# Performance work log

Measured on AMD Instinct MI355X. Metric: run time of the kernel, lower is better.

The kernel has to match this reference:

```python
import jax, jax.numpy as jnp
import numpy as np

B, N, T, N_IN = 4, 40, 64, 4
N_EMB, N_HID = 32, 64
EPS = 1e-05


def _spatial_rels(n):
    # fully-connected directed edges without self-loops (NRI convention)
    offdiag = np.ones((n, n)) - np.eye(n)
    recv_idx, send_idx = np.where(offdiag)[0], np.where(offdiag)[1]
    eye = np.eye(n, dtype=np.float32)
    return eye[recv_idx], eye[send_idx]  # [n*(n-1), n] each


def _temporal_rels(t):
    # all t*t ordered pairs (including self), one-hot
    eye = np.eye(t, dtype=np.float32)
    recv = np.repeat(np.arange(t), t)
    send = np.tile(np.arange(t), t)
    return eye[recv], eye[send]  # [t*t, t] each


def setup_inputs() -> dict:
    key = jax.random.key(0)
    ks = jax.random.split(key, 8)
    rel_rec, rel_send = _spatial_rels(N)
    rel_rec_t, rel_send_t = _temporal_rels(T)
    s_emb = 1.0 / np.sqrt(N_IN)
    s_lstm = 1.0 / np.sqrt(N_HID)
    s_att = 1.0 / np.sqrt(2 * N_HID)
    return {
        "inputs": jax.random.normal(ks[0], (B, N, T, N_IN), dtype=jnp.float32),
        "rel_rec": jnp.asarray(rel_rec),
        "rel_send": jnp.asarray(rel_send),
        "rel_rec_t": jnp.asarray(rel_rec_t),
        "rel_send_t": jnp.asarray(rel_send_t),
        "W_emb": jax.random.uniform(ks[1], (N_EMB, N_IN), jnp.float32, -s_emb, s_emb),
        "b_emb": jnp.zeros((N_EMB,), jnp.float32),
        "W_ih": jax.random.uniform(ks[2], (4 * N_HID, N_EMB), jnp.float32, -s_lstm, s_lstm),
        "W_hh": jax.random.uniform(ks[3], (4 * N_HID, N_HID), jnp.float32, -s_lstm, s_lstm),
        "b_ih": jax.random.uniform(ks[4], (4 * N_HID,), jnp.float32, -s_lstm, s_lstm),
        "b_hh": jax.random.uniform(ks[5], (4 * N_HID,), jnp.float32, -s_lstm, s_lstm),
        "W_att": jax.random.uniform(ks[6], (1, 2 * N_HID), jnp.float32, -s_att, s_att),
        "b_att": jnp.zeros((1,), jnp.float32),
    }


def _forward(inputs, rel_rec, rel_send, rel_rec_t, rel_send_t,
             W_emb, b_emb, W_ih, W_hh, b_ih, b_hh, W_att, b_att):
    b, n, t, _ = inputs.shape
    nh = W_hh.shape[1]
    locs = inputs[..., :2]

    # ---- LSTMEncoder: per-timestep embedding + LSTM cell (scan over time) ----
    emb = jnp.einsum("bnti,ei->bnte", inputs, W_emb) + b_emb       # [B,N,T,n_emb]
    xs = emb.transpose(2, 0, 1, 3).reshape(t, b * n, -1)            # [T,BN,n_emb]

    def step(carry, x):
        h, c = carry
        gates = x @ W_ih.T + b_ih + h @ W_hh.T + b_hh               # [BN,4H]
        i_g, f_g, g_g, o_g = jnp.split(gates, 4, axis=-1)           # torch gate order i,f,g,o
        i_g = jax.nn.sigmoid(i_g)
        f_g = jax.nn.sigmoid(f_g)
        g_g = jnp.tanh(g_g)
        o_g = jax.nn.sigmoid(o_g)
        c = f_g * c + i_g * g_g
        h = o_g * jnp.tanh(c)
        return (h, c), h

    h0 = jnp.zeros((b * n, nh), inputs.dtype)
    _, hs_t = jax.lax.scan(step, (h0, h0), xs)                      # [T,BN,H]
    hs = hs_t.transpose(1, 0, 2).reshape(b, n, t, nh)               # [B,N,T,H]

    # ---- SoftAttention over timesteps ----
    hsf = hs.reshape(b * n, t, nh)                                  # [BN,T,H]
    senders = jnp.einsum("kt,mth->mkh", rel_send_t, hsf)            # [BN,T*T,H]
    receivers = jnp.einsum("kt,mth->mkh", rel_rec_t, hsf)
    edges = jnp.concatenate([senders, receivers], axis=-1)          # [BN,T*T,2H]
    scores = jnp.einsum("mkf,of->mko", edges, W_att)[..., 0] + b_att[0]  # [BN,T*T]
    # adj = rel_send_t^T @ diag(scores) @ rel_rec_t (done without diag_embed)
    adj_s = jnp.einsum("ki,mk,kj->mij", rel_send_t, scores, rel_rec_t)   # [BN,T,T]
    adj_sn = jax.nn.softmax(adj_s, axis=-1)
    cs = jnp.einsum("mij,mjh->mih", adj_sn, hsf).reshape(b, n, t, nh)    # [B,N,T,H]

    # ---- HardwiredAttention over atoms ----
    locs_re = locs.reshape(b, n, -1)                                 # [B,N,T*2]
    snd = jnp.einsum("en,bnf->bef", rel_send, locs_re).reshape(b, -1, t, 2)
    rcv = jnp.einsum("en,bnf->bef", rel_rec, locs_re).reshape(b, -1, t, 2)
    dist = jnp.sqrt(((snd - rcv) ** 2).sum(-1))                      # [B,E,T]
    w = (1.0 / (dist + EPS)).transpose(0, 2, 1)                      # [B,T,E]
    adj_h = jnp.einsum("ei,bte,ej->btij", rel_send, w, rel_rec)      # [B,T,N,N]
    ch = jnp.einsum("btij,btjh->btih", adj_h, hs.transpose(0, 2, 1, 3))
    ch = ch.transpose(0, 2, 1, 3)                                    # [B,N,T,H]

    c_out = jnp.tanh(jnp.concatenate([cs[:, :, -1, :], ch.sum(2)], axis=-1))  # [B,N,2H]
    return c_out


def reference(inputs, rel_rec, rel_send, rel_rec_t, rel_send_t,
              W_emb, b_emb, W_ih, W_hh, b_ih, b_hh, W_att, b_att):
    return _forward(inputs, rel_rec, rel_send, rel_rec_t, rel_send_t,
                    W_emb, b_emb, W_ih, W_hh, b_ih, b_hh, W_att, b_att)
```

## Files before the change

kernel.cpp:

```cpp
#include <hip/hip_runtime.h>
#include <math.h>

#define BB   4
#define NN   40
#define TT   64
#define NIN  4
#define NEMB 32
#define NHID 64
#define EPSW 1e-5f

__device__ __forceinline__ float fast_sigmoid(float x) {
    return __fdividef(1.0f, 1.0f + __expf(-x));
}
__device__ __forceinline__ float fast_tanh(float x) {
    return __fdividef(2.0f, 1.0f + __expf(-2.0f * x)) - 1.0f;
}
__device__ __forceinline__ float lanebcast(float v, int l) {
    return __int_as_float(__builtin_amdgcn_readlane(__float_as_int(v), l));
}

__global__ __launch_bounds__(64, 1)
void k_lstm(const float* __restrict__ inputs,
            const float* __restrict__ W_emb,
            const float* __restrict__ b_emb,
            const float* __restrict__ W_ih,
            const float* __restrict__ W_hh,
            const float* __restrict__ b_ih,
            const float* __restrict__ b_hh,
            const float* __restrict__ W_att,
            float* __restrict__ out,
            float* __restrict__ hs_g)
{
    __shared__ __align__(16) float s_hs[TT * (NHID + 1)];
    __shared__ __align__(16) float s_war[NHID];
    __shared__ __align__(16) float s_p[TT];

    const int m = blockIdx.x;
    const int j = threadIdx.x;

    s_war[j] = W_att[NHID + j];

    const float4 xl = ((const float4*)(inputs + m * (TT * NIN)))[j];

    #define FOLD(PFX, ROW)                                                   \
        float PFX##0 = 0.f, PFX##1 = 0.f, PFX##2 = 0.f, PFX##3 = 0.f;        \
        float PFX##b = b_ih[ROW] + b_hh[ROW];                                \
        {                                                                    \
            const float4* wih4 = (const float4*)(W_ih + (ROW) * NEMB);       \
            _Pragma("unroll")                                                \
            for (int e4 = 0; e4 < NEMB / 4; ++e4) {                          \
                float4 wv = wih4[e4];                                        \
                const float4* wm = ((const float4*)W_emb) + 4 * e4;          \
                PFX##0 += wv.x*wm[0].x + wv.y*wm[1].x + wv.z*wm[2].x + wv.w*wm[3].x; \
                PFX##1 += wv.x*wm[0].y + wv.y*wm[1].y + wv.z*wm[2].y + wv.w*wm[3].y; \
                PFX##2 += wv.x*wm[0].z + wv.y*wm[1].z + wv.z*wm[2].z + wv.w*wm[3].z; \
                PFX##3 += wv.x*wm[0].w + wv.y*wm[1].w + wv.z*wm[2].w + wv.w*wm[3].w; \
                PFX##b += wv.x*b_emb[4*e4+0] + wv.y*b_emb[4*e4+1]            \
                        + wv.z*b_emb[4*e4+2] + wv.w*b_emb[4*e4+3];           \
            }                                                                \
        }
    FOLD(wcI, j)
    FOLD(wcF, NHID + j)
    FOLD(wcG, 2 * NHID + j)
    FOLD(wcO, 3 * NHID + j)
    #undef FOLD

    float4 wI[16], wF[16], wG[16], wO[16];
    {
        const float4* pI = (const float4*)(W_hh + (size_t)(j) * NHID);
        const float4* pF = (const float4*)(W_hh + (size_t)(NHID + j) * NHID);
        const float4* pG = (const float4*)(W_hh + (size_t)(2 * NHID + j) * NHID);
        const float4* pO = (const float4*)(W_hh + (size_t)(3 * NHID + j) * NHID);
        #pragma unroll
        for (int k = 0; k < 16; ++k) {
            wI[k] = pI[k]; wF[k] = pF[k]; wG[k] = pG[k]; wO[k] = pO[k];
        }
    }

    float c = 0.0f, h = 0.0f;
    #pragma unroll 1
    for (int t = 0; t < TT; ++t) {
        const float xb0 = lanebcast(xl.x, t);
        const float xb1 = lanebcast(xl.y, t);
        const float xb2 = lanebcast(xl.z, t);
        const float xb3 = lanebcast(xl.w, t);

        float aI0 = wcIb + xb0 * wcI0 + xb2 * wcI2;
        float aI1 = xb1 * wcI1 + xb3 * wcI3;
        float aF0 = wcFb + xb0 * wcF0 + xb2 * wcF2;
        float aF1 = xb1 * wcF1 + xb3 * wcF3;
        float aG0 = wcGb + xb0 * wcG0 + xb2 * wcG2;
        float aG1 = xb1 * wcG1 + xb3 * wcG3;
        float aO0 = wcOb + xb0 * wcO0 + xb2 * wcO2;
        float aO1 = xb1 * wcO1 + xb3 * wcO3;

        #pragma unroll
        for (int k = 0; k < 16; ++k) {
            const float h0 = lanebcast(h, 4 * k + 0);
            const float h1 = lanebcast(h, 4 * k + 1);
            const float h2 = lanebcast(h, 4 * k + 2);
            const float h3 = lanebcast(h, 4 * k + 3);
            aI0 += h0 * wI[k].x; aI1 += h1 * wI[k].y;
            aI0 += h2 * wI[k].z; aI1 += h3 * wI[k].w;
            aF0 += h0 * wF[k].x; aF1 += h1 * wF[k].y;
            aF0 += h2 * wF[k].z; aF1 += h3 * wF[k].w;
            aG0 += h0 * wG[k].x; aG1 += h1 * wG[k].y;
            aG0 += h2 * wG[k].z; aG1 += h3 * wG[k].w;
            aO0 += h0 * wO[k].x; aO1 += h1 * wO[k].y;
            aO0 += h2 * wO[k].z; aO1 += h3 * wO[k].w;
        }

        const float ig = fast_sigmoid(aI0 + aI1);
        const float fg = fast_sigmoid(aF0 + aF1);
        const float gg = fast_tanh(aG0 + aG1);
        const float og = fast_sigmoid(aO0 + aO1);
        c = fg * c + ig * gg;
        h = og * fast_tanh(c);
        s_hs[t * (NHID + 1) + j] = h;
    }
    __syncthreads();

    #pragma unroll 1
    for (int t = 0; t < TT; ++t)
        hs_g[m * (TT * NHID) + t * NHID + j] = s_hs[t * (NHID + 1) + j];

    {
        const int t = j;
        float r = 0.0f;
        #pragma unroll
        for (int k = 0; k < NHID; ++k)
            r += s_hs[t * (NHID + 1) + k] * s_war[k];
        float mx = r;
        #pragma unroll
        for (int off = 32; off >= 1; off >>= 1)
            mx = fmaxf(mx, __shfl_xor(mx, off));
        const float e = __expf(r - mx);
        float s = e;
        #pragma unroll
        for (int off = 32; off >= 1; off >>= 1)
            s += __shfl_xor(s, off);
        s_p[t] = __fdividef(e, s);
    }
    __syncthreads();

    {
        float acc = 0.0f;
        #pragma unroll
        for (int t = 0; t < TT; ++t)
            acc += s_p[t] * s_hs[t * (NHID + 1) + j];
        out[m * (2 * NHID) + j] = fast_tanh(acc);
    }
}

__global__ __launch_bounds__(256)
void k_spatial(const float* __restrict__ inputs,
               const float* __restrict__ hs_g,
               float* __restrict__ out)
{
    __shared__ float s_w[TT * NN];
    __shared__ float s_part[4 * NHID];

    const int bi  = blockIdx.x;
    const int b   = bi / NN;
    const int i   = bi - b * NN;
    const int tid = threadIdx.x;

    for (int idx = tid; idx < TT * NN; idx += 256) {
        const int t = idx / NN;
        const int j = idx - t * NN;
        const float* pi = inputs + ((b * NN + i) * TT + t) * NIN;
        const float* pj = inputs + ((b * NN + j) * TT + t) * NIN;
        const float dx = pi[0] - pj[0];
        const float dy = pi[1] - pj[1];
        const float d  = sqrtf(dx * dx + dy * dy);
        s_w[idx] = (j == i) ? 0.0f : __fdividef(1.0f, d + EPSW);
    }
    __syncthreads();

    const int h = tid & 63;
    const int q = tid >> 6;

    const float* base = hs_g + (size_t)b * NN * TT * NHID + h;
    float a0 = 0.f, a1 = 0.f, a2 = 0.f, a3 = 0.f;
    for (int t = q * 16; t < q * 16 + 16; ++t) {
        const float* hp = base + t * NHID;
        const float* wp = s_w + t * NN;
        #pragma unroll
        for (int j = 0; j < NN; j += 4) {
            a0 += wp[j + 0] * hp[(size_t)(j + 0) * TT * NHID];
            a1 += wp[j + 1] * hp[(size_t)(j + 1) * TT * NHID];
            a2 += wp[j + 2] * hp[(size_t)(j + 2) * TT * NHID];
            a3 += wp[j + 3] * hp[(size_t)(j + 3) * TT * NHID];
        }
    }
    s_part[q * NHID + h] = (a0 + a1) + (a2 + a3);
    __syncthreads();

    if (tid < NHID) {
        const float s = s_part[tid] + s_part[NHID + tid] +
                        s_part[2 * NHID + tid] + s_part[3 * NHID + tid];
        out[bi * (2 * NHID) + NHID + tid] = fast_tanh(s);
    }
}

extern "C" void kernel_launch(void* const* d_in, const int* in_sizes, int n_in,
                              void* d_out, int out_size, void* d_ws, size_t ws_size,
                              hipStream_t stream) {
    const float* inputs = (const float*)d_in[0];
    const float* W_emb  = (const float*)d_in[5];
    const float* b_emb  = (const float*)d_in[6];
    const float* W_ih   = (const float*)d_in[7];
    const float* W_hh   = (const float*)d_in[8];
    const float* b_ih   = (const float*)d_in[9];
    const float* b_hh   = (const float*)d_in[10];
    const float* W_att  = (const float*)d_in[11];

    float* outp = (float*)d_out;
    float* hs_g = (float*)d_ws;

    hipLaunchKernelGGL(k_lstm, dim3(BB * NN), dim3(64), 0, stream,
                       inputs, W_emb, b_emb, W_ih, W_hh, b_ih, b_hh, W_att,
                       outp, hs_g);
    hipLaunchKernelGGL(k_spatial, dim3(BB * NN), dim3(256), 0, stream,
                       inputs, hs_g, outp);
}
```

Baseline: 158.4 us.

## Use packed fp16 dot2 with hi/lo split for LSTM recurrent matvec

Stores the recurrent W_hh weights as packed fp16 pairs and computes the per-step matvec with v_dot2 instructions. The hidden state is split into an fp16 high part and a residual, each packed in pairs, which halves the number of readlane broadcasts per pass and uses two dot2 passes in place of four scalar FMAs. It also writes hidden states to global memory inside the time loop instead of in a separate copy loop. Weight values are rounded to fp16, which loses some precision, and the extra shuffles and packing sit on the serial recurrence path.

```diff
diff --git a/kernel.cpp b/kernel.cpp
--- a/kernel.cpp
+++ b/kernel.cpp
@@ -9,6 +9,8 @@
 #define NHID 64
 #define EPSW 1e-5f
 
+typedef __fp16 half2v __attribute__((ext_vector_type(2)));
+
 __device__ __forceinline__ float fast_sigmoid(float x) {
     return __fdividef(1.0f, 1.0f + __expf(-x));
 }
@@ -17,6 +19,15 @@
 }
 __device__ __forceinline__ float lanebcast(float v, int l) {
     return __int_as_float(__builtin_amdgcn_readlane(__float_as_int(v), l));
+}
+__device__ __forceinline__ half2v i2h2(int v) {
+    union { int i; half2v h; } u; u.i = v; return u.h;
+}
+__device__ __forceinline__ int h22i(half2v v) {
+    union { int i; half2v h; } u; u.h = v; return u.i;
+}
+__device__ __forceinline__ half2v pack_rne(float a, float b) {
+    half2v r; r.x = (__fp16)a; r.y = (__fp16)b; return r;
 }
 
 __global__ __launch_bounds__(64, 1)
@@ -65,7 +76,7 @@
     FOLD(wcO, 3 * NHID + j)
     #undef FOLD
 
-    float4 wI[16], wF[16], wG[16], wO[16];
+    half2v wI[32], wF[32], wG[32], wO[32];
     {
         const float4* pI = (const float4*)(W_hh + (size_t)(j) * NHID);
         const float4* pF = (const float4*)(W_hh + (size_t)(NHID + j) * NHID);
@@ -73,9 +84,15 @@
         const float4* pO = (const float4*)(W_hh + (size_t)(3 * NHID + j) * NHID);
         #pragma unroll
         for (int k = 0; k < 16; ++k) {
-            wI[k] = pI[k]; wF[k] = pF[k]; wG[k] = pG[k]; wO[k] = pO[k];
-        }
-    }
+            float4 q;
+            q = pI[k]; wI[2*k] = pack_rne(q.x, q.y); wI[2*k+1] = pack_rne(q.z, q.w);
+            q = pF[k]; wF[2*k] = pack_rne(q.x, q.y); wF[2*k+1] = pack_rne(q.z, q.w);
+            q = pG[k]; wG[2*k] = pack_rne(q.x, q.y); wG[2*k+1] = pack_rne(q.z, q.w);
+            q = pO[k]; wO[2*k] = pack_rne(q.x, q.y); wO[2*k+1] = pack_rne(q.z, q.w);
+        }
+    }
+
+    float* hs_out = hs_g + (size_t)m * (TT * NHID) + j;
 
     float c = 0.0f, h = 0.0f;
     #pragma unroll 1
@@ -84,7 +101,6 @@
         const float xb1 = lanebcast(xl.y, t);
         const float xb2 = lanebcast(xl.z, t);
         const float xb3 = lanebcast(xl.w, t);
-
         float aI0 = wcIb + xb0 * wcI0 + xb2 * wcI2;
         float aI1 = xb1 * wcI1 + xb3 * wcI3;
         float aF0 = wcFb + xb0 * wcF0 + xb2 * wcF2;
@@ -94,20 +110,47 @@
         float aO0 = wcOb + xb0 * wcO0 + xb2 * wcO2;
         float aO1 = xb1 * wcO1 + xb3 * wcO3;
 
-        #pragma unroll
-        for (int k = 0; k < 16; ++k) {
-            const float h0 = lanebcast(h, 4 * k + 0);
-            const float h1 = lanebcast(h, 4 * k + 1);
-            const float h2 = lanebcast(h, 4 * k + 2);
-            const float h3 = lanebcast(h, 4 * k + 3);
-            aI0 += h0 * wI[k].x; aI1 += h1 * wI[k].y;
-            aI0 += h2 * wI[k].z; aI1 += h3 * wI[k].w;
-            aF0 += h0 * wF[k].x; aF1 += h1 * wF[k].y;
-            aF0 += h2 * wF[k].z; aF1 += h3 * wF[k].w;
-            aG0 += h0 * wG[k].x; aG1 += h1 * wG[k].y;
-            aG0 += h2 * wG[k].z; aG1 += h3 * wG[k].w;
-            aO0 += h0 * wO[k].x; aO1 += h1 * wO[k].y;
-            aO0 += h2 * wO[k].z; aO1 += h3 * wO[k].w;
+        const float h16f = (float)(__fp16)h;
+        const float e    = h - h16f;
+        const float hnb  = __shfl_xor(h, 1);
+        const float enb  = __shfl_xor(e, 1);
+        const int hpi = h22i(pack_rne(h, hnb));
+        const int epi = h22i(pack_rne(e, enb));
+
+        int hb[32];
+        #pragma unroll
+        for (int k = 0; k < 32; ++k)
+            hb[k] = __builtin_amdgcn_readlane(hpi, 2 * k);
+        #pragma unroll
+        for (int k = 0; k < 32; k += 2) {
+            const half2v h0 = i2h2(hb[k]);
+            const half2v h1 = i2h2(hb[k + 1]);
+            aI0 = __builtin_amdgcn_fdot2(h0, wI[k],     aI0, false);
+            aI1 = __builtin_amdgcn_fdot2(h1, wI[k + 1], aI1, false);
+            aF0 = __builtin_amdgcn_fdot2(h0, wF[k],     aF0, false);
+            aF1 = __builtin_amdgcn_fdot2(h1, wF[k + 1], aF1, false);
+            aG0 = __builtin_amdgcn_fdot2(h0, wG[k],     aG0, false);
+            aG1 = __builtin_amdgcn_fdot2(h1, wG[k + 1], aG1, false);
+            aO0 = __builtin_amdgcn_fdot2(h0, wO[k],     aO0, false);
+            aO1 = __builtin_amdgcn_fdot2(h1, wO[k + 1], aO1, false);
+        }
+
+        int eb[32];
+        #pragma unroll
+        for (int k = 0; k < 32; ++k)
+            eb[k] = __builtin_amdgcn_readlane(epi, 2 * k);
+        #pragma unroll
+        for (int k = 0; k < 32; k += 2) {
+            const half2v e0 = i2h2(eb[k]);
+            const half2v e1 = i2h2(eb[k + 1]);
+            aI0 = __builtin_amdgcn_fdot2(e0, wI[k],     aI0, false);
+            aI1 = __builtin_amdgcn_fdot2(e1, wI[k + 1], aI1, false);
+            aF0 = __builtin_amdgcn_fdot2(e0, wF[k],     aF0, false);
+            aF1 = __builtin_amdgcn_fdot2(e1, wF[k + 1], aF1, false);
+            aG0 = __builtin_amdgcn_fdot2(e0, wG[k],     aG0, false);
+            aG1 = __builtin_amdgcn_fdot2(e1, wG[k + 1], aG1, false);
+            aO0 = __builtin_amdgcn_fdot2(e0, wO[k],     aO0, false);
+            aO1 = __builtin_amdgcn_fdot2(e1, wO[k + 1], aO1, false);
         }
 
         const float ig = fast_sigmoid(aI0 + aI1);
@@ -117,12 +160,9 @@
         c = fg * c + ig * gg;
         h = og * fast_tanh(c);
         s_hs[t * (NHID + 1) + j] = h;
-    }
-    __syncthreads();
-
-    #pragma unroll 1
-    for (int t = 0; t < TT; ++t)
-        hs_g[m * (TT * NHID) + t * NHID + j] = s_hs[t * (NHID + 1) + j];
+        hs_out[t * NHID] = h;
+    }
+    __syncthreads();
 
     {
         const int t = j;
```

New measurement: 156.6 us. No clear change (-1.1%).
